# Kernel optimization log

Measured on AMD Instinct MI355X. Metric: run time of the kernel, lower is better.

## Reference

```python
import jax, jax.numpy as jnp
import numpy as np

NUM_CODES = 4096
EMBED_DIM = 256
N_TOKENS = 65536
COMMITMENT_COST = 0.1


def setup_inputs() -> dict:
    key = jax.random.key(0)
    k1, k2 = jax.random.split(key)
    z_e = jax.random.normal(k1, (N_TOKENS, EMBED_DIM), dtype=jnp.float32)
    embeddings = jax.random.normal(k2, (NUM_CODES, EMBED_DIM), dtype=jnp.float32)
    return {"z_e": z_e, "embeddings": embeddings}


def reference(z_e, embeddings):
    # Squared Euclidean distances (argmin-equivalent to torch.cdist):
    # d2[n,k] = |z_n|^2 - 2 z_n.E_k + |E_k|^2
    z_sq = jnp.sum(z_e * z_e, axis=-1, keepdims=True)          # [N,1]
    e_sq = jnp.sum(embeddings * embeddings, axis=-1)            # [K]
    d2 = z_sq - 2.0 * (z_e @ embeddings.T) + e_sq[None, :]      # [N,K]
    indices = jnp.argmin(d2, axis=-1)                           # [N] int

    z_q = embeddings[indices]                                   # [N,D] gather

    # commitment loss: mse(detach(z_q), z_e)
    diff = jax.lax.stop_gradient(z_q) - z_e
    commitment_loss = COMMITMENT_COST * jnp.mean(diff * diff)

    # straight-through estimator
    z_q_st = z_e + jax.lax.stop_gradient(z_q - z_e)

    # perplexity from code usage histogram (avoids materializing one-hot)
    counts = jnp.zeros((NUM_CODES,), dtype=jnp.float32).at[indices].add(1.0)
    avg_probs = counts / z_e.shape[0]
    perplexity = jnp.exp(-jnp.sum(avg_probs * jnp.log(avg_probs + 1e-10)))

    return z_q_st, indices, commitment_loss, perplexity
```

## Files before the change

### kernel.cpp

```cpp
#include <hip/hip_runtime.h>

#define N_TOKENS   65536
#define NUM_CODES  4096
#define EMBED_DIM  256

#define IDX_OFF  ((size_t)N_TOKENS * EMBED_DIM)
#define LOSS_OFF (IDX_OFF + N_TOKENS)

#define DELTA 0.2f
#define UCAP  16384
#define RT    8

typedef _Float16 half8 __attribute__((ext_vector_type(8)));
typedef float    f32x4 __attribute__((ext_vector_type(4)));
typedef unsigned long long u64;


__device__ __forceinline__ void gl_lds16(const void* g, void* l) {
    __builtin_amdgcn_global_load_lds(
        (const __attribute__((address_space(1))) unsigned int*)g,
        (__attribute__((address_space(3))) unsigned int*)l, 16, 0, 0);
}

__global__ void k_conv(const float* __restrict__ X, _Float16* __restrict__ Xh, int nrows) {
    int gid = blockIdx.x * 256 + threadIdx.x;
    int n  = gid >> 5;
    int kg = gid & 31;
    if (n >= nrows) return;
    const float* src = X + (size_t)n * EMBED_DIM + kg * 8;
    float4 a = *(const float4*)src;
    float4 b = *(const float4*)(src + 4);
    int tb = n >> 7, r = n & 127, kc = kg >> 2, g = kg & 3;
    int gp = g ^ ((r >> 1) & 3);
    half8 hv;
    hv[0]=(_Float16)a.x; hv[1]=(_Float16)a.y; hv[2]=(_Float16)a.z; hv[3]=(_Float16)a.w;
    hv[4]=(_Float16)b.x; hv[5]=(_Float16)b.y; hv[6]=(_Float16)b.z; hv[7]=(_Float16)b.w;
    *(half8*)(Xh + (size_t)tb * 32768 + kc * 4096 + r * 32 + gp * 8) = hv;
}

__global__ void k_esq(const float* __restrict__ E, float* __restrict__ esq) {
    int k = blockIdx.x;
    int l = threadIdx.x;
    float4 v = *(const float4*)(E + (size_t)k * EMBED_DIM + l * 4);
    float s = v.x * v.x + v.y * v.y + v.z * v.z + v.w * v.w;
    #pragma unroll
    for (int off = 32; off; off >>= 1) s += __shfl_down(s, off, 64);
    if (l == 0) esq[k] = s;
}

__global__ void k_transpose(const float* __restrict__ E, float* __restrict__ Et) {
    __shared__ float t[32][33];
    int tx = threadIdx.x & 31, ty = threadIdx.x >> 5;
    int c0 = blockIdx.x * 32, d0 = blockIdx.y * 32;
    #pragma unroll
    for (int i = 0; i < 4; ++i)
        t[ty + 8 * i][tx] = E[(size_t)(c0 + ty + 8 * i) * EMBED_DIM + d0 + tx];
    __syncthreads();
    #pragma unroll
    for (int i = 0; i < 4; ++i)
        Et[(size_t)(d0 + ty + 8 * i) * NUM_CODES + c0 + tx] = t[tx][ty + 8 * i];
}

__launch_bounds__(256, 2)
__global__ void k_argmin_mfma(const _Float16* __restrict__ Zh, const _Float16* __restrict__ Eh,
                              const float* __restrict__ esq, int* __restrict__ out_idx,
                              int* __restrict__ ulist, int* __restrict__ ucount) {
    __shared__ __align__(16) _Float16 As[4096];
    __shared__ __align__(16) _Float16 Bs[4096];

    const int tid  = threadIdx.x;
    const int lane = tid & 63;
    const int w    = tid >> 6;
    const int w0   = w >> 1;
    const int w1   = w & 1;
    const int l15  = lane & 15;
    const int q    = lane >> 4;
    const int tb   = blockIdx.x;

    int aoff[4], boff[4];
    #pragma unroll
    for (int i = 0; i < 4; ++i) {
        int r = w0 * 64 + i * 16 + l15;
        aoff[i] = r * 64 + ((q ^ ((r >> 1) & 3)) * 16);
    }
    #pragma unroll
    for (int j = 0; j < 4; ++j) {
        int c = w1 * 64 + j * 16 + l15;
        boff[j] = c * 64 + ((q ^ ((c >> 1) & 3)) * 16);
    }

    float best[16], sec[16];
    int   bidx[16];
    #pragma unroll
    for (int k = 0; k < 16; ++k) { best[k] = 1e30f; sec[k] = 1e30f; bidx[k] = 0; }

    const _Float16* Zt = Zh + (size_t)tb * 32768;

    for (int it = 0; it < 32; ++it) {
        const _Float16* Et = Eh + (size_t)it * 32768;
        f32x4 acc[4][4];
        #pragma unroll
        for (int i = 0; i < 4; ++i)
            #pragma unroll
            for (int j = 0; j < 4; ++j) acc[i][j] = (f32x4)0.0f;

        for (int kc = 0; kc < 8; ++kc) {
            __syncthreads();
            const _Float16* ga = Zt + kc * 4096 + w * 1024 + lane * 8;
            const _Float16* gb = Et + kc * 4096 + w * 1024 + lane * 8;
            gl_lds16(ga,       As + w * 1024);
            gl_lds16(ga + 512, As + w * 1024 + 512);
            gl_lds16(gb,       Bs + w * 1024);
            gl_lds16(gb + 512, Bs + w * 1024 + 512);
            __syncthreads();

            half8 af[4], bf[4];
            #pragma unroll
            for (int i = 0; i < 4; ++i)
                af[i] = *(const half8*)((const char*)As + aoff[i]);
            #pragma unroll
            for (int j = 0; j < 4; ++j)
                bf[j] = *(const half8*)((const char*)Bs + boff[j]);
            #pragma unroll
            for (int i = 0; i < 4; ++i)
                #pragma unroll
                for (int j = 0; j < 4; ++j)
                    acc[i][j] = __builtin_amdgcn_mfma_f32_16x16x32_f16(af[i], bf[j], acc[i][j], 0, 0, 0);
        }

        int cbase = it * 128 + w1 * 64 + l15;
        #pragma unroll
        for (int j = 0; j < 4; ++j) {
            float e  = esq[cbase + j * 16];
            int code = cbase + j * 16;
            #pragma unroll
            for (int i = 0; i < 4; ++i)
                #pragma unroll
                for (int r = 0; r < 4; ++r) {
                    float v = fmaf(-2.0f, acc[i][j][r], e);
                    int k = i * 4 + r;
                    float ob = best[k];
                    bool t = v < ob;
                    best[k] = t ? v : ob;
                    sec[k]  = fminf(sec[k], t ? ob : v);
                    bidx[k] = t ? code : bidx[k];
                }
        }
    }

    #pragma unroll
    for (int m = 1; m <= 8; m <<= 1) {
        #pragma unroll
        for (int k = 0; k < 16; ++k) {
            float ob = __shfl_xor(best[k], m, 64);
            float os = __shfl_xor(sec[k],  m, 64);
            int   oi = __shfl_xor(bidx[k], m, 64);
            float ns = fminf(fminf(sec[k], os), fmaxf(best[k], ob));
            bool t = (ob < best[k]) || (ob == best[k] && oi < bidx[k]);
            best[k] = t ? ob : best[k];
            bidx[k] = t ? oi : bidx[k];
            sec[k]  = ns;
        }
    }

    __syncthreads();
    float* mb = (float*)As;
    float* ms = mb + 256;
    int*   mi = (int*)(mb + 512);
    if (l15 == 0) {
        #pragma unroll
        for (int k = 0; k < 16; ++k) {
            int row = w0 * 64 + (k >> 2) * 16 + q * 4 + (k & 3);
            mb[row * 2 + w1] = best[k];
            ms[row * 2 + w1] = sec[k];
            mi[row * 2 + w1] = bidx[k];
        }
    }
    __syncthreads();
    if (tid < 128) {
        float b0 = mb[tid * 2], b1 = mb[tid * 2 + 1];
        float s0 = ms[tid * 2], s1 = ms[tid * 2 + 1];
        int   i0 = mi[tid * 2], i1 = mi[tid * 2 + 1];
        bool t = (b1 < b0) || (b1 == b0 && i1 < i0);
        float bb = t ? b1 : b0;
        int   ii = t ? i1 : i0;
        float ss = fminf(fminf(s0, s1), fmaxf(b0, b1));
        int token = tb * 128 + tid;
        out_idx[token] = ii;
        if (ss - bb < DELTA) {
            int p = atomicAdd(ucount, 1);
            if (p < UCAP) ulist[p] = token;
        }
    }
}

__launch_bounds__(256)
__global__ void k_refine(const float* __restrict__ Z, const float* __restrict__ Et,
                         const float* __restrict__ esq, const int* __restrict__ ulist,
                         const int* __restrict__ ucount, u64* __restrict__ umin) {
    int cnt = *ucount; if (cnt > UCAP) cnt = UCAP;
    const int g   = blockIdx.x >> 2;
    const int qtr = blockIdx.x & 3;
    if (g * RT >= cnt) return;

    __shared__ float zs[RT][256];
    const int tid  = threadIdx.x;
    const int lane = tid & 63;

    #pragma unroll
    for (int t = 0; t < RT; ++t) {
        int u = g * RT + t;
        int tok = ulist[(u < cnt) ? u : g * RT];
        zs[t][tid] = Z[(size_t)tok * EMBED_DIM + tid];
    }
    __syncthreads();

    const int c0 = qtr * 1024 + tid * 4;
    f32x4 acc[RT];
    #pragma unroll
    for (int t = 0; t < RT; ++t) acc[t] = (f32x4)0.0f;

    for (int d4 = 0; d4 < 64; ++d4) {
        f32x4 e0 = *(const f32x4*)(Et + (size_t)(d4 * 4 + 0) * NUM_CODES + c0);
        f32x4 e1 = *(const f32x4*)(Et + (size_t)(d4 * 4 + 1) * NUM_CODES + c0);
        f32x4 e2 = *(const f32x4*)(Et + (size_t)(d4 * 4 + 2) * NUM_CODES + c0);
        f32x4 e3 = *(const f32x4*)(Et + (size_t)(d4 * 4 + 3) * NUM_CODES + c0);
        #pragma unroll
        for (int t = 0; t < RT; ++t) {
            f32x4 z4 = *(const f32x4*)&zs[t][d4 * 4];
            acc[t] += z4.x * e0;
            acc[t] += z4.y * e1;
            acc[t] += z4.z * e2;
            acc[t] += z4.w * e3;
        }
    }

    f32x4 eq = *(const f32x4*)(esq + c0);
    #pragma unroll
    for (int t = 0; t < RT; ++t) {
        u64 p = ~0ull;
        #pragma unroll
        for (int r = 0; r < 4; ++r) {
            float v = fmaf(-2.0f, acc[t][r], eq[r]) + 4096.0f;
            u64 cand = ((u64)__float_as_uint(v) << 32) | (unsigned)(c0 + r);
            p = cand < p ? cand : p;
        }
        #pragma unroll
        for (int m = 1; m <= 32; m <<= 1) {
            u64 o = __shfl_xor(p, m, 64);
            p = o < p ? o : p;
        }
        int u = g * RT + t;
        if (lane == 0 && u < cnt) atomicMin(umin + u, p);
    }
}

__global__ void k_rwrite(const int* __restrict__ ulist, const int* __restrict__ ucount,
                         const u64* __restrict__ umin, int* __restrict__ out_idx) {
    int cnt = *ucount; if (cnt > UCAP) cnt = UCAP;
    int u = blockIdx.x * 256 + threadIdx.x;
    if (u < cnt) out_idx[ulist[u]] = (int)(umin[u] & 0xFFFFFFFFu);
}

__global__ void k_gather(const float* __restrict__ Z, const float* __restrict__ E,
                         float* __restrict__ out,
                         float* __restrict__ loss_parts, unsigned* __restrict__ hist) {
    int wave = threadIdx.x >> 6, lane = threadIdx.x & 63;
    int token = blockIdx.x * 4 + wave;
    int* idxi = (int*)(out + IDX_OFF);
    int k = idxi[token];
    float4 z = *(const float4*)(Z + (size_t)token * EMBED_DIM + lane * 4);
    float4 qv = *(const float4*)(E + (size_t)k * EMBED_DIM + lane * 4);
    *(float4*)(out + (size_t)token * EMBED_DIM + lane * 4) = qv;
    float dx = qv.x - z.x, dy = qv.y - z.y, dz = qv.z - z.z, dw = qv.w - z.w;
    float s = dx * dx + dy * dy + dz * dz + dw * dw;
    #pragma unroll
    for (int off = 32; off; off >>= 1) s += __shfl_down(s, off, 64);
    if (lane == 0) {
        atomicAdd(loss_parts + (blockIdx.x & 1023), s);
        atomicAdd(hist + k, 1u);
        out[IDX_OFF + token] = (float)k;
    }
}

__global__ void k_final(const float* __restrict__ loss_parts,
                        const unsigned* __restrict__ hist, float* __restrict__ out) {
    __shared__ float red[256];
    int t = threadIdx.x;
    float s = 0.0f;
    for (int i = t; i < 1024; i += 256) s += loss_parts[i];
    red[t] = s;
    __syncthreads();
    #pragma unroll
    for (int off = 128; off; off >>= 1) {
        if (t < off) red[t] += red[t + off];
        __syncthreads();
    }
    float loss = 0.1f * red[0] / (float)(N_TOKENS * EMBED_DIM);

    float h = 0.0f;
    for (int i = t; i < NUM_CODES; i += 256) {
        float p = (float)hist[i] / (float)N_TOKENS;
        h += p * logf(p + 1e-10f);
    }
    __syncthreads();
    red[t] = h;
    __syncthreads();
    #pragma unroll
    for (int off = 128; off; off >>= 1) {
        if (t < off) red[t] += red[t + off];
        __syncthreads();
    }
    if (t == 0) {
        out[LOSS_OFF]     = loss;
        out[LOSS_OFF + 1] = expf(-red[0]);
    }
}

extern "C" void kernel_launch(void* const* d_in, const int* in_sizes, int n_in,
                              void* d_out, int out_size, void* d_ws, size_t ws_size,
                              hipStream_t stream) {
    const float* Z = (const float*)d_in[0];
    const float* E = (const float*)d_in[1];
    float* out = (float*)d_out;
    char*  ob  = (char*)d_out;
    char*  ws  = (char*)d_ws;

    _Float16* Zh = (_Float16*)ob;
    _Float16* Eh = (_Float16*)(ob + 33554432);
    float*    Et = (float*)(ob + 33554432 + 2097152);
    u64*      umin = (u64*)(ob + 33554432 + 2097152 + 4194304);
    int*      idx = (int*)(out + IDX_OFF);

    float*    esq        = (float*)ws;
    int*      ulist      = (int*)(ws + 16384);
    int*      ucount     = (int*)(ws + 81920);
    float*    loss_parts = (float*)(ws + 81984);
    unsigned* hist       = (unsigned*)(ws + 86080);

    hipMemsetAsync(ws + 81920, 0, 64 + 4096 + 16384, stream);
    hipMemsetAsync(umin, 0xFF, (size_t)UCAP * 8, stream);

    k_conv       <<<(N_TOKENS * 32) / 256, 256, 0, stream>>>(Z, Zh, N_TOKENS);
    k_conv       <<<(NUM_CODES * 32) / 256, 256, 0, stream>>>(E, Eh, NUM_CODES);
    k_esq        <<<NUM_CODES, 64, 0, stream>>>(E, esq);
    k_transpose  <<<dim3(NUM_CODES / 32, EMBED_DIM / 32), 256, 0, stream>>>(E, Et);
    k_argmin_mfma<<<N_TOKENS / 128, 256, 0, stream>>>(Zh, Eh, esq, idx, ulist, ucount);
    k_refine     <<<4 * (UCAP / RT), 256, 0, stream>>>(Z, Et, esq, ulist, ucount, umin);
    k_rwrite     <<<UCAP / 256, 256, 0, stream>>>(ulist, ucount, umin, idx);
    k_gather     <<<N_TOKENS / 4, 256, 0, stream>>>(Z, E, out, loss_parts, hist);
    k_final      <<<1, 256, 0, stream>>>(loss_parts, hist, out);
}
```

Measured before the change: 399.2 us.

## Keep Z tile in registers as fp16 fragments and stream only codebook tiles

The separate Z fp32-to-fp16 conversion kernel is dropped. Each wave now loads its 64 token rows straight from fp32 global memory, converts them in registers and holds all A fragments (32 half8 values) for the whole kernel. The codebook is pre-swizzled into MFMA lane order, so 64-code tiles stream into LDS and are read without a bank-conflict swizzle, and the code norms are cached in LDS. This removes a full Z conversion pass and the repeated A loads through LDS, at the cost of much higher register pressure under a 2-block occupancy target and a synchronization before every 64-code tile.

Measured after the change: 344.6 us. 13.7% less time.

```diff
diff --git a/kernel.cpp b/kernel.cpp
--- a/kernel.cpp
+++ b/kernel.cpp
@@ -14,7 +14,6 @@
 typedef _Float16 half8 __attribute__((ext_vector_type(8)));
 typedef float    f32x4 __attribute__((ext_vector_type(4)));
 typedef unsigned long long u64;
-
 
 __device__ __forceinline__ void gl_lds16(const void* g, void* l) {
     __builtin_amdgcn_global_load_lds(
@@ -22,20 +21,19 @@
         (__attribute__((address_space(3))) unsigned int*)l, 16, 0, 0);
 }
 
-__global__ void k_conv(const float* __restrict__ X, _Float16* __restrict__ Xh, int nrows) {
+__global__ void k_convE(const float* __restrict__ E, _Float16* __restrict__ Eh) {
     int gid = blockIdx.x * 256 + threadIdx.x;
     int n  = gid >> 5;
     int kg = gid & 31;
-    if (n >= nrows) return;
-    const float* src = X + (size_t)n * EMBED_DIM + kg * 8;
+    const float* src = E + (size_t)n * EMBED_DIM + kg * 8;
     float4 a = *(const float4*)src;
     float4 b = *(const float4*)(src + 4);
-    int tb = n >> 7, r = n & 127, kc = kg >> 2, g = kg & 3;
-    int gp = g ^ ((r >> 1) & 3);
+    int ct = n >> 4, l15 = n & 15, kc = kg >> 2, q = kg & 3;
+    int lane = q * 16 + l15;
     half8 hv;
     hv[0]=(_Float16)a.x; hv[1]=(_Float16)a.y; hv[2]=(_Float16)a.z; hv[3]=(_Float16)a.w;
     hv[4]=(_Float16)b.x; hv[5]=(_Float16)b.y; hv[6]=(_Float16)b.z; hv[7]=(_Float16)b.w;
-    *(half8*)(Xh + (size_t)tb * 32768 + kc * 4096 + r * 32 + gp * 8) = hv;
+    *(half8*)(Eh + ((size_t)(ct * 8 + kc) * 64 + lane) * 8) = hv;
 }
 
 __global__ void k_esq(const float* __restrict__ E, float* __restrict__ esq) {
@@ -62,11 +60,11 @@
 }
 
 __launch_bounds__(256, 2)
-__global__ void k_argmin_mfma(const _Float16* __restrict__ Zh, const _Float16* __restrict__ Eh,
+__global__ void k_argmin_mfma(const float* __restrict__ Z, const _Float16* __restrict__ Eh,
                               const float* __restrict__ esq, int* __restrict__ out_idx,
                               int* __restrict__ ulist, int* __restrict__ ucount) {
-    __shared__ __align__(16) _Float16 As[4096];
-    __shared__ __align__(16) _Float16 Bs[4096];
+    __shared__ __align__(16) _Float16 Bs[16384];
+    __shared__ float esq_s[NUM_CODES];
 
     const int tid  = threadIdx.x;
     const int lane = tid & 63;
@@ -77,16 +75,22 @@
     const int q    = lane >> 4;
     const int tb   = blockIdx.x;
 
-    int aoff[4], boff[4];
-    #pragma unroll
-    for (int i = 0; i < 4; ++i) {
-        int r = w0 * 64 + i * 16 + l15;
-        aoff[i] = r * 64 + ((q ^ ((r >> 1) & 3)) * 16);
-    }
-    #pragma unroll
-    for (int j = 0; j < 4; ++j) {
-        int c = w1 * 64 + j * 16 + l15;
-        boff[j] = c * 64 + ((q ^ ((c >> 1) & 3)) * 16);
+    for (int i = tid; i < NUM_CODES; i += 256) esq_s[i] = esq[i];
+
+    half8 A[4][8];
+    const float* Zb = Z + ((size_t)tb * 128 + w0 * 64) * EMBED_DIM;
+    #pragma unroll
+    for (int rt = 0; rt < 4; ++rt) {
+        const float* Zr = Zb + (rt * 16 + l15) * EMBED_DIM + q * 8;
+        #pragma unroll
+        for (int kc = 0; kc < 8; ++kc) {
+            float4 a = *(const float4*)(Zr + kc * 32);
+            float4 b = *(const float4*)(Zr + kc * 32 + 4);
+            half8 hv;
+            hv[0]=(_Float16)a.x; hv[1]=(_Float16)a.y; hv[2]=(_Float16)a.z; hv[3]=(_Float16)a.w;
+            hv[4]=(_Float16)b.x; hv[5]=(_Float16)b.y; hv[6]=(_Float16)b.z; hv[7]=(_Float16)b.w;
+            A[rt][kc] = hv;
+        }
     }
 
     float best[16], sec[16];
@@ -94,51 +98,42 @@
     #pragma unroll
     for (int k = 0; k < 16; ++k) { best[k] = 1e30f; sec[k] = 1e30f; bidx[k] = 0; }
 
-    const _Float16* Zt = Zh + (size_t)tb * 32768;
-
-    for (int it = 0; it < 32; ++it) {
-        const _Float16* Et = Eh + (size_t)it * 32768;
-        f32x4 acc[4][4];
-        #pragma unroll
-        for (int i = 0; i < 4; ++i)
+    const int cb = w1 * 2;
+
+    for (int it = 0; it < NUM_CODES / 64; ++it) {
+        __syncthreads();
+        const _Float16* src = Eh + (size_t)it * 16384 + (w * 8) * 512 + lane * 8;
+        #pragma unroll
+        for (int s = 0; s < 8; ++s)
+            gl_lds16(src + s * 512, Bs + (w * 8 + s) * 512);
+        __syncthreads();
+
+        f32x4 acc[4][2];
+        #pragma unroll
+        for (int rt = 0; rt < 4; ++rt) { acc[rt][0] = (f32x4)0.0f; acc[rt][1] = (f32x4)0.0f; }
+
+        #pragma unroll
+        for (int kc = 0; kc < 8; ++kc) {
+            half8 bf0 = *(const half8*)(Bs + ((cb + 0) * 8 + kc) * 512 + lane * 8);
+            half8 bf1 = *(const half8*)(Bs + ((cb + 1) * 8 + kc) * 512 + lane * 8);
             #pragma unroll
-            for (int j = 0; j < 4; ++j) acc[i][j] = (f32x4)0.0f;
-
-        for (int kc = 0; kc < 8; ++kc) {
-            __syncthreads();
-            const _Float16* ga = Zt + kc * 4096 + w * 1024 + lane * 8;
-            const _Float16* gb = Et + kc * 4096 + w * 1024 + lane * 8;
-            gl_lds16(ga,       As + w * 1024);
-            gl_lds16(ga + 512, As + w * 1024 + 512);
-            gl_lds16(gb,       Bs + w * 1024);
-            gl_lds16(gb + 512, Bs + w * 1024 + 512);
-            __syncthreads();
-
-            half8 af[4], bf[4];
+            for (int rt = 0; rt < 4; ++rt) {
+                acc[rt][0] = __builtin_amdgcn_mfma_f32_16x16x32_f16(A[rt][kc], bf0, acc[rt][0], 0, 0, 0);
+                acc[rt][1] = __builtin_amdgcn_mfma_f32_16x16x32_f16(A[rt][kc], bf1, acc[rt][1], 0, 0, 0);
+            }
+        }
+
+        int code0 = it * 64 + cb * 16 + l15;
+        #pragma unroll
+        for (int c = 0; c < 2; ++c) {
+            float e  = esq_s[code0 + c * 16];
+            int code = code0 + c * 16;
             #pragma unroll
-            for (int i = 0; i < 4; ++i)
-                af[i] = *(const half8*)((const char*)As + aoff[i]);
-            #pragma unroll
-            for (int j = 0; j < 4; ++j)
-                bf[j] = *(const half8*)((const char*)Bs + boff[j]);
-            #pragma unroll
-            for (int i = 0; i < 4; ++i)
-                #pragma unroll
-                for (int j = 0; j < 4; ++j)
-                    acc[i][j] = __builtin_amdgcn_mfma_f32_16x16x32_f16(af[i], bf[j], acc[i][j], 0, 0, 0);
-        }
-
-        int cbase = it * 128 + w1 * 64 + l15;
-        #pragma unroll
-        for (int j = 0; j < 4; ++j) {
-            float e  = esq[cbase + j * 16];
-            int code = cbase + j * 16;
-            #pragma unroll
-            for (int i = 0; i < 4; ++i)
+            for (int rt = 0; rt < 4; ++rt)
                 #pragma unroll
                 for (int r = 0; r < 4; ++r) {
-                    float v = fmaf(-2.0f, acc[i][j][r], e);
-                    int k = i * 4 + r;
+                    float v = fmaf(-2.0f, acc[rt][c][r], e);
+                    int k = rt * 4 + r;
                     float ob = best[k];
                     bool t = v < ob;
                     best[k] = t ? v : ob;
@@ -164,7 +159,7 @@
     }
 
     __syncthreads();
-    float* mb = (float*)As;
+    float* mb = (float*)Bs;
     float* ms = mb + 256;
     int*   mi = (int*)(mb + 512);
     if (l15 == 0) {
@@ -326,11 +321,10 @@
     char*  ob  = (char*)d_out;
     char*  ws  = (char*)d_ws;
 
-    _Float16* Zh = (_Float16*)ob;
-    _Float16* Eh = (_Float16*)(ob + 33554432);
-    float*    Et = (float*)(ob + 33554432 + 2097152);
-    u64*      umin = (u64*)(ob + 33554432 + 2097152 + 4194304);
-    int*      idx = (int*)(out + IDX_OFF);
+    _Float16* Eh   = (_Float16*)(ob + 50331648);
+    float*    Et   = (float*)(ob + 54525952);
+    u64*      umin = (u64*)(ob + 58720256);
+    int*      idx  = (int*)(out + IDX_OFF);
 
     float*    esq        = (float*)ws;
     int*      ulist      = (int*)(ws + 16384);
@@ -341,11 +335,10 @@
     hipMemsetAsync(ws + 81920, 0, 64 + 4096 + 16384, stream);
     hipMemsetAsync(umin, 0xFF, (size_t)UCAP * 8, stream);
 
-    k_conv       <<<(N_TOKENS * 32) / 256, 256, 0, stream>>>(Z, Zh, N_TOKENS);
-    k_conv       <<<(NUM_CODES * 32) / 256, 256, 0, stream>>>(E, Eh, NUM_CODES);
+    k_convE      <<<(NUM_CODES * 32) / 256, 256, 0, stream>>>(E, Eh);
     k_esq        <<<NUM_CODES, 64, 0, stream>>>(E, esq);
     k_transpose  <<<dim3(NUM_CODES / 32, EMBED_DIM / 32), 256, 0, stream>>>(E, Et);
-    k_argmin_mfma<<<N_TOKENS / 128, 256, 0, stream>>>(Zh, Eh, esq, idx, ulist, ucount);
+    k_argmin_mfma<<<N_TOKENS / 128, 256, 0, stream>>>(Z, Eh, esq, idx, ulist, ucount);
     k_refine     <<<4 * (UCAP / RT), 256, 0, stream>>>(Z, Et, esq, ulist, ucount, umin);
     k_rwrite     <<<UCAP / 256, 256, 0, stream>>>(ulist, ucount, umin, idx);
     k_gather     <<<N_TOKENS / 4, 256, 0, stream>>>(Z, E, out, loss_parts, hist);
```
